# Performance work log

Hardware: AMD Instinct MI355X
Metric: run time of the kernel (lower is better)

## Reference

```python
import jax, jax.numpy as jnp
import numpy as np

D_MODEL = 128
D_STATE = 16
D_CONV = 2
EXPAND = 2
D_INNER = EXPAND * D_MODEL  # 256
DT_RANK = (D_MODEL + 15) // 16  # 8
GROUPS = 4
EPS = 1e-5


def setup_inputs() -> dict:
    key = jax.random.key(0)
    ks = jax.random.split(key, 12)
    s = lambda k, shape, sc=0.02: jax.random.normal(k, shape, dtype=jnp.float32) * sc
    inp = {
        "x_hsi": jax.random.normal(ks[0], (8, D_MODEL, 64, 64), dtype=jnp.float32),
        "W_in": s(ks[1], (D_MODEL, 2 * D_INNER)),            # in_proj (no bias)
        "conv_w": s(ks[2], (D_INNER, D_CONV), 0.5),          # depthwise causal conv, k=2
        "conv_b": s(ks[3], (D_INNER,), 0.1),
        "W_x": s(ks[4], (D_INNER, DT_RANK + 2 * D_STATE)),   # x_proj (no bias)
        "W_dt": s(ks[5], (DT_RANK, D_INNER), 0.1),
        "b_dt": s(ks[6], (D_INNER,), 0.1),
        "A_log": jnp.log(jnp.broadcast_to(jnp.arange(1, D_STATE + 1, dtype=jnp.float32), (D_INNER, D_STATE))),
        "D": jnp.ones((D_INNER,), dtype=jnp.float32),
        "W_out": s(ks[7], (D_INNER, D_MODEL)),               # out_proj (no bias)
        "gn_gamma": jnp.ones((D_MODEL,), dtype=jnp.float32),
        "gn_beta": jnp.zeros((D_MODEL,), dtype=jnp.float32),
    }
    return inp


def _causal_conv_k2(x, w, b):
    # x: [B, L, Din]; w: [Din, 2]; causal depthwise conv, kernel size 2
    xp = jnp.pad(x, ((0, 0), (1, 0), (0, 0)))
    return xp[:, :-1] * w[:, 0] + xp[:, 1:] * w[:, 1] + b


def _selective_scan(xc, dt, Bmat, Cmat, A, D):
    # xc,dt: [B,L,Din]; Bmat,Cmat: [B,L,N]; A: [Din,N]; D: [Din]
    def step(h, inp):
        dt_t, B_t, C_t, x_t = inp          # [B,Din],[B,N],[B,N],[B,Din]
        dA = jnp.exp(dt_t[..., None] * A)                      # [B,Din,N]
        dBx = dt_t[..., None] * B_t[:, None, :] * x_t[..., None]
        h = dA * h + dBx
        y = jnp.einsum('bdn,bn->bd', h, C_t)
        return h, y

    B_, L, Din = xc.shape
    h0 = jnp.zeros((B_, Din, A.shape[1]), dtype=xc.dtype)
    xs = (jnp.swapaxes(dt, 0, 1), jnp.swapaxes(Bmat, 0, 1),
          jnp.swapaxes(Cmat, 0, 1), jnp.swapaxes(xc, 0, 1))
    _, ys = jax.lax.scan(step, h0, xs)     # ys: [L,B,Din]
    return jnp.swapaxes(ys, 0, 1) + xc * D


def _mamba(x, W_in, conv_w, conv_b, W_x, W_dt, b_dt, A_log, D, W_out):
    # x: [B, L, d_model]
    xz = x @ W_in                                   # [B,L,2*Din]
    xh, z = jnp.split(xz, 2, axis=-1)
    xh = jax.nn.silu(_causal_conv_k2(xh, conv_w, conv_b))
    x_dbl = xh @ W_x                                # [B,L,dt_rank+2N]
    dt_low = x_dbl[..., :DT_RANK]
    Bmat = x_dbl[..., DT_RANK:DT_RANK + D_STATE]
    Cmat = x_dbl[..., DT_RANK + D_STATE:]
    dt = jax.nn.softplus(dt_low @ W_dt + b_dt)      # [B,L,Din]
    A = -jnp.exp(A_log)
    y = _selective_scan(xh, dt, Bmat, Cmat, A, D)
    y = y * jax.nn.silu(z)
    return y @ W_out


def _group_norm(x, gamma, beta):
    # x: [B,C,H,W]
    B_, C, H, W = x.shape
    xr = x.reshape(B_, GROUPS, -1)
    mean = xr.mean(-1, keepdims=True)
    var = xr.var(-1, keepdims=True)
    xn = ((xr - mean) * jax.lax.rsqrt(var + EPS)).reshape(B_, C, H, W)
    return xn * gamma[:, None, None] + beta[:, None, None]


def reference(x_hsi, W_in, conv_w, conv_b, W_x, W_dt, b_dt, A_log, D, W_out, gn_gamma, gn_beta):
    B_, C, H, W = x_hsi.shape
    x = jnp.transpose(x_hsi, (0, 2, 3, 1)).reshape(B_, H * W, C)
    x = _mamba(x, W_in, conv_w, conv_b, W_x, W_dt, b_dt, A_log, D, W_out)
    x = jnp.transpose(x.reshape(B_, H, W, C), (0, 3, 1, 2))
    x = jax.nn.silu(_group_norm(x, gn_gamma, gn_beta))
    return x + x_hsi
```

## Files before the change

kernel.cpp:

```cpp
#include <hip/hip_runtime.h>
#include <hip/hip_bf16.h>
#include <math.h>

#define BATCH   8
#define LSEQ    4096
#define CMODEL  128
#define DIN     256
#define NSTATE  16
#define RRANK   8
#define NCH     128
#define TCH     32

typedef __attribute__((ext_vector_type(8))) short short8;
typedef __attribute__((ext_vector_type(4))) float f32x4;
typedef __attribute__((ext_vector_type(2))) float f32x2;

__device__ __forceinline__ float sigmoid_fast(float x) {
    return __builtin_amdgcn_rcpf(1.0f + __expf(-x));
}
__device__ __forceinline__ float silu_fast(float x) { return x * sigmoid_fast(x); }
__device__ __forceinline__ float softplus_fast(float x) {
    return fmaxf(x, 0.0f) + __logf(1.0f + __expf(-fabsf(x)));
}
__device__ __forceinline__ unsigned short f2bf(float f) {
    unsigned u = __float_as_uint(f);
    return (unsigned short)((u + 0x7FFFu + ((u >> 16) & 1u)) >> 16);
}
__device__ __forceinline__ float bf2f(unsigned short u) {
    return __uint_as_float(((unsigned)u) << 16);
}
__device__ __forceinline__ unsigned pk2bf(float a, float b) {
    __hip_bfloat162 t = __float22bfloat162_rn(make_float2(a, b));
    unsigned r;
    __builtin_memcpy(&r, &t, 4);
    return r;
}

__device__ __forceinline__ void dA_powers(float dtv, const float* A, bool fast,
                                          float* dA)
{
    if (fast) {
        float e1 = __expf(dtv * A[0]);
        float e2 = e1 * e1;
        float e4 = e2 * e2;
        float e8 = e4 * e4;
        dA[0] = e1;        dA[1] = e2;        dA[2] = e2 * e1;   dA[3] = e4;
        dA[4] = e4 * e1;   dA[5] = e4 * e2;   dA[6] = e4 * dA[2]; dA[7] = e8;
        dA[8] = e8 * e1;   dA[9] = e8 * e2;   dA[10] = e8 * dA[2]; dA[11] = e8 * e4;
        dA[12] = e8 * dA[4]; dA[13] = e8 * dA[5]; dA[14] = e8 * dA[6]; dA[15] = e8 * e8;
    } else {
        #pragma unroll
        for (int n = 0; n < 16; ++n) dA[n] = __expf(dtv * A[n]);
    }
}

#define LSTR 72

__device__ __forceinline__ void tr64_bf(const float* __restrict__ src, int lds,
                                        int r0, int c0,
                                        unsigned short* __restrict__ dst, int ldd)
{
    __shared__ float ts[64][65];
    const int tid = threadIdx.x;
    #pragma unroll
    for (int it = 0; it < 4; ++it) {
        int slot = tid + it * 256;
        int i = slot >> 4, j4 = slot & 15;
        float4 v = *(const float4*)&src[(size_t)(r0 + i) * lds + c0 + j4 * 4];
        ts[i][j4*4+0] = v.x; ts[i][j4*4+1] = v.y;
        ts[i][j4*4+2] = v.z; ts[i][j4*4+3] = v.w;
    }
    __syncthreads();
    #pragma unroll
    for (int it = 0; it < 4; ++it) {
        int slot = tid + it * 256;
        int row = slot >> 4, c4 = slot & 15;
        unsigned p0 = pk2bf(ts[c4*4+0][row], ts[c4*4+1][row]);
        unsigned p1 = pk2bf(ts[c4*4+2][row], ts[c4*4+3][row]);
        unsigned long long u = (unsigned long long)p0 | ((unsigned long long)p1 << 32);
        *(unsigned long long*)&dst[(size_t)(c0 + row) * ldd + r0 + c4 * 4] = u;
    }
}

__global__ __launch_bounds__(256) void k0_setup(
    const float* __restrict__ W_in, const float* __restrict__ W_out,
    unsigned short* __restrict__ wtin, unsigned short* __restrict__ wtout,
    float* __restrict__ part)
{
    const int bid = blockIdx.x;
    if (bid < 16) {
        int ct = bid >> 3, jt = bid & 7;
        tr64_bf(W_in, 512, ct * 64, jt * 64, wtin, 128);
    } else if (bid < 24) {
        int t3 = bid - 16;
        int kt = t3 >> 1, ct = t3 & 1;
        tr64_bf(W_out, 128, kt * 64, ct * 64, wtout, 256);
    } else {
        if (threadIdx.x < 64) part[threadIdx.x] = 0.0f;
    }
}

__global__ __launch_bounds__(512) void k1_gemm_in(
    const float* __restrict__ x_hsi, const unsigned short* __restrict__ wtin,
    float* __restrict__ xh_raw, float* __restrict__ z_silu)
{
    __shared__ __align__(16) unsigned short Abf[128 * LSTR];
    __shared__ __align__(16) unsigned short Bbf[256 * LSTR];
    const int tid = threadIdx.x;
    const int R0  = blockIdx.x * 128;
    const int b   = R0 >> 12;
    const int l0  = R0 & 4095;
    const int jbase = blockIdx.y * 256;

    const int w    = tid >> 6;
    const int lane = tid & 63;
    const int lm   = lane & 15;
    const int q    = lane >> 4;
    const int mbase = (w & 1) * 64;
    const int nbase = (w >> 1) * 64;

    f32x4 acc[4][4];
    #pragma unroll
    for (int i = 0; i < 4; ++i)
        #pragma unroll
        for (int j = 0; j < 4; ++j) acc[i][j] = (f32x4){0.f, 0.f, 0.f, 0.f};

    const int cq = tid & 15;
    const int lq = tid >> 4;

    for (int kc = 0; kc < 128; kc += 64) {
        __syncthreads();
        {
            float v[4][4];
            #pragma unroll
            for (int t = 0; t < 4; ++t) {
                float4 f = *(const float4*)&x_hsi[((b * 128 + kc + cq * 4 + t) << 12) + l0 + lq * 4];
                v[t][0] = f.x; v[t][1] = f.y; v[t][2] = f.z; v[t][3] = f.w;
            }
            #pragma unroll
            for (int i = 0; i < 4; ++i) {
                unsigned p0 = pk2bf(v[0][i], v[1][i]);
                unsigned p1 = pk2bf(v[2][i], v[3][i]);
                unsigned long long u = (unsigned long long)p0 | ((unsigned long long)p1 << 32);
                *(unsigned long long*)&Abf[(lq * 4 + i) * LSTR + cq * 4] = u;
            }
        }
        #pragma unroll
        for (int it = 0; it < 4; ++it) {
            int slot = tid + it * 512;
            int r = slot >> 3, seg = slot & 7;
            short8 vb = *(const short8*)&wtin[(size_t)(jbase + r) * 128 + kc + seg * 8];
            *(short8*)&Bbf[r * LSTR + seg * 8] = vb;
        }
        __syncthreads();
        #pragma unroll
        for (int kt = 0; kt < 2; ++kt) {
            short8 af[4], bfr[4];
            #pragma unroll
            for (int mt = 0; mt < 4; ++mt)
                af[mt] = *(const short8*)&Abf[(mbase + mt * 16 + lm) * LSTR + kt * 32 + q * 8];
            #pragma unroll
            for (int nt = 0; nt < 4; ++nt)
                bfr[nt] = *(const short8*)&Bbf[(nbase + nt * 16 + lm) * LSTR + kt * 32 + q * 8];
            #pragma unroll
            for (int mt = 0; mt < 4; ++mt)
                #pragma unroll
                for (int nt = 0; nt < 4; ++nt)
                    acc[mt][nt] = __builtin_amdgcn_mfma_f32_16x16x32_bf16(
                        af[mt], bfr[nt], acc[mt][nt], 0, 0, 0);
        }
    }

    const bool is_xh = (jbase == 0);
    #pragma unroll
    for (int mt = 0; mt < 4; ++mt) {
        #pragma unroll
        for (int r = 0; r < 4; ++r) {
            int row = R0 + mbase + mt * 16 + q * 4 + r;
            #pragma unroll
            for (int nt = 0; nt < 4; ++nt) {
                int col = nbase + nt * 16 + lm;
                float val = acc[mt][nt][r];
                if (is_xh) xh_raw[row * 256 + col] = val;
                else       z_silu[row * 256 + col] = silu_fast(val);
            }
        }
    }
}

__global__ __launch_bounds__(256) void k4_xdbl(
    const float* __restrict__ xh_raw, const float* __restrict__ conv_w,
    const float* __restrict__ conv_b, const float* __restrict__ W_x,
    float* __restrict__ xdbl, unsigned short* __restrict__ xcbf)
{
    __shared__ float xcs[128][68];
    __shared__ float wxs[64 * 40];
    __shared__ float cw0[256], cw1[256], cbs[256];
    const int tid = threadIdx.x;
    cw0[tid] = conv_w[2 * tid];
    cw1[tid] = conv_w[2 * tid + 1];
    cbs[tid] = conv_b[tid];

    const int R0 = blockIdx.x * 128;
    const int tc = tid & 7;
    const int tr = tid >> 3;

    float acc[4][5];
    #pragma unroll
    for (int i = 0; i < 4; ++i)
        #pragma unroll
        for (int j = 0; j < 5; ++j) acc[i][j] = 0.0f;

    for (int kc = 0; kc < 256; kc += 64) {
        __syncthreads();
        #pragma unroll
        for (int it = 0; it < 3; ++it) {
            int i4 = tid + it * 256;
            if (i4 < 640) ((float4*)wxs)[i4] = ((const float4*)&W_x[kc * 40])[i4];
        }
        #pragma unroll
        for (int it = 0; it < 8; ++it) {
            int idx = tid + it * 256;
            int r = idx >> 4, qq = idx & 15;
            int row = R0 + r;
            float4 cur = *(const float4*)&xh_raw[row * 256 + kc + qq * 4];
            float4 prv = make_float4(0.f, 0.f, 0.f, 0.f);
            if ((row & 4095) != 0)
                prv = *(const float4*)&xh_raw[(row - 1) * 256 + kc + qq * 4];
            int d = kc + qq * 4;
            float4 o;
            o.x = silu_fast(prv.x * cw0[d+0] + cur.x * cw1[d+0] + cbs[d+0]);
            o.y = silu_fast(prv.y * cw0[d+1] + cur.y * cw1[d+1] + cbs[d+1]);
            o.z = silu_fast(prv.z * cw0[d+2] + cur.z * cw1[d+2] + cbs[d+2]);
            o.w = silu_fast(prv.w * cw0[d+3] + cur.w * cw1[d+3] + cbs[d+3]);
            *(float4*)&xcs[r][qq * 4] = o;
            unsigned p0 = pk2bf(o.x, o.y), p1 = pk2bf(o.z, o.w);
            unsigned long long u = (unsigned long long)p0 | ((unsigned long long)p1 << 32);
            *(unsigned long long*)&xcbf[(size_t)row * 256 + d] = u;
        }
        __syncthreads();
        #pragma unroll 2
        for (int k = 0; k < 64; ++k) {
            float wv[5];
            #pragma unroll
            for (int j = 0; j < 5; ++j) wv[j] = wxs[k * 40 + tc * 5 + j];
            #pragma unroll
            for (int i = 0; i < 4; ++i) {
                float a = xcs[tr * 4 + i][k];
                #pragma unroll
                for (int j = 0; j < 5; ++j) acc[i][j] = fmaf(a, wv[j], acc[i][j]);
            }
        }
    }
    #pragma unroll
    for (int i = 0; i < 4; ++i) {
        int row = R0 + tr * 4 + i;
        #pragma unroll
        for (int j = 0; j < 5; ++j) xdbl[row * 40 + tc * 5 + j] = acc[i][j];
    }
}

__global__ __launch_bounds__(256) void k6_scan1(
    const unsigned short* __restrict__ xcbf, const float* __restrict__ xdbl,
    const float* __restrict__ W_dt, const float* __restrict__ b_dt,
    const float* __restrict__ A_log,
    float* __restrict__ hend, float* __restrict__ dtsg,
    float* __restrict__ dtvg)
{
    __shared__ float xd[TCH * 40];
    const int d = threadIdx.x;
    const int chunk = blockIdx.x;
    const int b = blockIdx.y;
    const int t0 = b * LSEQ + chunk * TCH;

    {
        const float4* src = (const float4*)&xdbl[t0 * 40];
        if (d < 256) ((float4*)xd)[d] = src[d];
        int i2 = d + 256;
        if (i2 < 320) ((float4*)xd)[i2] = src[i2];
    }

    float A[16];
    #pragma unroll
    for (int qq = 0; qq < 4; ++qq) {
        float4 al = *(const float4*)&A_log[d * 16 + qq * 4];
        A[qq*4+0] = -__expf(al.x); A[qq*4+1] = -__expf(al.y);
        A[qq*4+2] = -__expf(al.z); A[qq*4+3] = -__expf(al.w);
    }
    bool fast = true;
    #pragma unroll
    for (int n = 1; n < 16; ++n)
        fast = fast && (fabsf(A[n] - (n + 1) * A[0]) <= 1e-4f * fabsf(A[n]) + 1e-7f);

    float wdt[8];
    #pragma unroll
    for (int r = 0; r < 8; ++r) wdt[r] = W_dt[r * 256 + d];
    const float bdt = b_dt[d];

    f32x2 h2[8];
    #pragma unroll
    for (int j = 0; j < 8; ++j) h2[j] = (f32x2){0.f, 0.f};
    float dtsum = 0.f;
    __syncthreads();

    #pragma unroll 2
    for (int tt = 0; tt < TCH; ++tt) {
        const int row = t0 + tt;
        float xcv = bf2f(xcbf[(size_t)row * 256 + d]);

        const float* xr = &xd[tt * 40];
        float dl[8];
        *(float4*)&dl[0] = *(const float4*)&xr[0];
        *(float4*)&dl[4] = *(const float4*)&xr[4];
        float dtr = bdt;
        #pragma unroll
        for (int r = 0; r < 8; ++r) dtr = fmaf(dl[r], wdt[r], dtr);
        float dtv = softplus_fast(dtr);
        dtsum += dtv;
        float dtx = dtv * xcv;
        dtvg[(size_t)row * 256 + d] = dtv;

        float Bt[16] __attribute__((aligned(16)));
        #pragma unroll
        for (int qq = 0; qq < 4; ++qq)
            *(float4*)&Bt[qq * 4] = *(const float4*)&xr[8 + qq * 4];

        float dA[16] __attribute__((aligned(16)));
        dA_powers(dtv, A, fast, dA);
        const f32x2* dA2 = (const f32x2*)dA;
        const f32x2* Bt2 = (const f32x2*)Bt;
        f32x2 dtx2 = (f32x2){dtx, dtx};
        #pragma unroll
        for (int j = 0; j < 8; ++j)
            h2[j] = dA2[j] * h2[j] + dtx2 * Bt2[j];
    }

    const float* hf = (const float*)h2;
    const int base = ((b * NCH + chunk) * 256 + d) * 16;
    #pragma unroll
    for (int qq = 0; qq < 4; ++qq)
        *(float4*)&hend[base + qq * 4] = make_float4(hf[qq*4], hf[qq*4+1], hf[qq*4+2], hf[qq*4+3]);
    dtsg[(b * NCH + chunk) * 256 + d] = dtsum;
}

__global__ __launch_bounds__(256) void k7_combine(
    const float* __restrict__ dtsg, const float* __restrict__ A_log,
    float* __restrict__ hx)
{
    const int idx = blockIdx.x * 256 + threadIdx.x;
    const int b = idx >> 12;
    const int rem = idx & 4095;
    const int d = rem >> 4, n = rem & 15;
    const float An = -__expf(A_log[d * 16 + n]);
    const int base = b * NCH * 4096 + rem;
    const int sbase = b * NCH * 256 + d;
    float h = 0.f;
    float Sb[8], Eb[8];
    #pragma unroll
    for (int j = 0; j < 8; ++j) {
        Sb[j] = dtsg[sbase + j * 256];
        Eb[j] = hx[base + j * 4096];
    }
    for (int g = 0; g < NCH / 8; ++g) {
        const int o  = base + g * 32768;
        const int so = sbase + g * 2048;
        float Sn[8] = {0,0,0,0,0,0,0,0}, En[8] = {0,0,0,0,0,0,0,0};
        if (g < NCH / 8 - 1) {
            #pragma unroll
            for (int j = 0; j < 8; ++j) {
                Sn[j] = dtsg[so + 2048 + j * 256];
                En[j] = hx[o + 32768 + j * 4096];
            }
        }
        #pragma unroll
        for (int j = 0; j < 8; ++j) {
            hx[o + j * 4096] = h;
            float P = __expf(Sb[j] * An);
            h = fmaf(P, h, Eb[j]);
        }
        #pragma unroll
        for (int j = 0; j < 8; ++j) { Sb[j] = Sn[j]; Eb[j] = En[j]; }
    }
}

__global__ __launch_bounds__(256) void k8_scan2(
    const unsigned short* __restrict__ xcbf, const float* __restrict__ xdbl,
    const float* __restrict__ dtvg, const float* __restrict__ A_log,
    const float* __restrict__ Dvec, const float* __restrict__ hin,
    const float* __restrict__ zsilu, unsigned short* __restrict__ ybf)
{
    __shared__ float xd[TCH * 40];
    const int d = threadIdx.x;
    const int chunk = blockIdx.x;
    const int b = blockIdx.y;
    const int t0 = b * LSEQ + chunk * TCH;

    {
        const float4* src = (const float4*)&xdbl[t0 * 40];
        if (d < 256) ((float4*)xd)[d] = src[d];
        int i2 = d + 256;
        if (i2 < 320) ((float4*)xd)[i2] = src[i2];
    }

    float A[16];
    #pragma unroll
    for (int qq = 0; qq < 4; ++qq) {
        float4 al = *(const float4*)&A_log[d * 16 + qq * 4];
        A[qq*4+0] = -__expf(al.x); A[qq*4+1] = -__expf(al.y);
        A[qq*4+2] = -__expf(al.z); A[qq*4+3] = -__expf(al.w);
    }
    bool fast = true;
    #pragma unroll
    for (int n = 1; n < 16; ++n)
        fast = fast && (fabsf(A[n] - (n + 1) * A[0]) <= 1e-4f * fabsf(A[n]) + 1e-7f);

    const float Dd = Dvec[d];

    f32x2 h2[8];
    const int hbase = ((b * NCH + chunk) * 256 + d) * 16;
    {
        float hf[16];
        #pragma unroll
        for (int qq = 0; qq < 4; ++qq) {
            float4 hv = *(const float4*)&hin[hbase + qq * 4];
            hf[qq*4+0] = hv.x; hf[qq*4+1] = hv.y; hf[qq*4+2] = hv.z; hf[qq*4+3] = hv.w;
        }
        #pragma unroll
        for (int j = 0; j < 8; ++j) h2[j] = (f32x2){hf[2*j], hf[2*j+1]};
    }
    __syncthreads();

    #pragma unroll 2
    for (int tt = 0; tt < TCH; ++tt) {
        const int row = t0 + tt;
        const size_t gi = (size_t)row * 256 + d;
        float dtv = dtvg[gi];
        float xcv = bf2f(xcbf[gi]);
        float dtx = dtv * xcv;

        const float* xr = &xd[tt * 40];
        float Bt[16] __attribute__((aligned(16)));
        float Ct[16] __attribute__((aligned(16)));
        #pragma unroll
        for (int qq = 0; qq < 4; ++qq) {
            *(float4*)&Bt[qq * 4] = *(const float4*)&xr[8 + qq * 4];
            *(float4*)&Ct[qq * 4] = *(const float4*)&xr[24 + qq * 4];
        }

        float dA[16] __attribute__((aligned(16)));
        dA_powers(dtv, A, fast, dA);
        const f32x2* dA2 = (const f32x2*)dA;
        const f32x2* Bt2 = (const f32x2*)Bt;
        const f32x2* Ct2 = (const f32x2*)Ct;
        f32x2 dtx2 = (f32x2){dtx, dtx};
        f32x2 yv2 = (f32x2){0.f, 0.f};
        #pragma unroll
        for (int j = 0; j < 8; ++j) {
            h2[j] = dA2[j] * h2[j] + dtx2 * Bt2[j];
            yv2 = yv2 + h2[j] * Ct2[j];
        }
        float yv = yv2.x + yv2.y;
        yv = fmaf(Dd, xcv, yv);
        ybf[gi] = f2bf(yv * zsilu[gi]);
    }
}

__global__ __launch_bounds__(256) void k9_gemm_out(
    const unsigned short* __restrict__ ybf, const unsigned short* __restrict__ wtout,
    unsigned short* __restrict__ out_bf, float* __restrict__ part)
{
    __shared__ __align__(16) unsigned short Abf[128 * LSTR];
    __shared__ __align__(16) unsigned short Bbf[128 * LSTR];
    const int tid = threadIdx.x;
    const int R0 = blockIdx.x * 128;
    const int b  = R0 >> 12;
    const int l0 = R0 & 4095;

    const int w    = tid >> 6;
    const int lane = tid & 63;
    const int lm   = lane & 15;
    const int q    = lane >> 4;
    const int mbase = (w & 1) * 64;
    const int nbase = (w >> 1) * 64;

    f32x4 acc[4][4];
    #pragma unroll
    for (int i = 0; i < 4; ++i)
        #pragma unroll
        for (int j = 0; j < 4; ++j) acc[i][j] = (f32x4){0.f, 0.f, 0.f, 0.f};

    for (int kc = 0; kc < 256; kc += 64) {
        __syncthreads();
        #pragma unroll
        for (int it = 0; it < 4; ++it) {
            int slot = tid + it * 256;
            int r = slot >> 3, seg = slot & 7;
            short8 va = *(const short8*)&wtout[(size_t)r * 256 + kc + seg * 8];
            *(short8*)&Abf[r * LSTR + seg * 8] = va;
            short8 vb = *(const short8*)&ybf[(size_t)(R0 + r) * 256 + kc + seg * 8];
            *(short8*)&Bbf[r * LSTR + seg * 8] = vb;
        }
        __syncthreads();
        #pragma unroll
        for (int kt = 0; kt < 2; ++kt) {
            short8 af[4], bfr[4];
            #pragma unroll
            for (int mt = 0; mt < 4; ++mt)
                af[mt] = *(const short8*)&Abf[(mbase + mt * 16 + lm) * LSTR + kt * 32 + q * 8];
            #pragma unroll
            for (int nt = 0; nt < 4; ++nt)
                bfr[nt] = *(const short8*)&Bbf[(nbase + nt * 16 + lm) * LSTR + kt * 32 + q * 8];
            #pragma unroll
            for (int mt = 0; mt < 4; ++mt)
                #pragma unroll
                for (int nt = 0; nt < 4; ++nt)
                    acc[mt][nt] = __builtin_amdgcn_mfma_f32_16x16x32_bf16(
                        af[mt], bfr[nt], acc[mt][nt], 0, 0, 0);
        }
    }

    #pragma unroll
    for (int mt = 0; mt < 4; ++mt) {
        #pragma unroll
        for (int r = 0; r < 4; ++r) {
            int c = mbase + mt * 16 + q * 4 + r;
            long base = (long)(b * 128 + c) * 4096 + l0;
            #pragma unroll
            for (int nt = 0; nt < 4; ++nt)
                out_bf[base + nbase + nt * 16 + lm] = f2bf(acc[mt][nt][r]);
        }
    }

    float s0 = 0.f, q0 = 0.f, s1 = 0.f, q1 = 0.f;
    #pragma unroll
    for (int mt = 0; mt < 4; ++mt)
        #pragma unroll
        for (int nt = 0; nt < 4; ++nt)
            #pragma unroll
            for (int r = 0; r < 4; ++r) {
                float v = acc[mt][nt][r];
                if (mt < 2) { s0 += v; q0 += v * v; }
                else        { s1 += v; q1 += v * v; }
            }
    #pragma unroll
    for (int off = 32; off > 0; off >>= 1) {
        s0 += __shfl_down(s0, off, 64);
        q0 += __shfl_down(q0, off, 64);
        s1 += __shfl_down(s1, off, 64);
        q1 += __shfl_down(q1, off, 64);
    }
    if (lane == 0) {
        int g0 = mbase >> 5;
        atomicAdd(&part[(b * 4 + g0) * 2],     s0);
        atomicAdd(&part[(b * 4 + g0) * 2 + 1], q0);
        atomicAdd(&part[(b * 4 + g0 + 1) * 2],     s1);
        atomicAdd(&part[(b * 4 + g0 + 1) * 2 + 1], q1);
    }
}

__global__ __launch_bounds__(256) void k10c_apply(
    const unsigned short* __restrict__ out_bf, const float* __restrict__ part,
    const float* __restrict__ gamma, const float* __restrict__ beta,
    const float* __restrict__ x_hsi, float* __restrict__ out)
{
    __shared__ float sstat[64];
    if (threadIdx.x < 32) {
        float S = part[threadIdx.x * 2];
        float Q = part[threadIdx.x * 2 + 1];
        const float inv_n = 1.0f / 131072.0f;
        float mean = S * inv_n;
        float var  = Q * inv_n - mean * mean;
        sstat[threadIdx.x * 2]     = mean;
        sstat[threadIdx.x * 2 + 1] = rsqrtf(var + 1e-5f);
    }
    __syncthreads();
    const int idx4 = blockIdx.x * 256 + threadIdx.x;
    const int flat = idx4 * 4;
    const int c = (flat >> 12) & 127;
    const int b = flat >> 19;
    const int g = c >> 5;
    const float mean = sstat[(b * 4 + g) * 2];
    const float inv  = sstat[(b * 4 + g) * 2 + 1];
    const float ga = gamma[c], be = beta[c];
    ushort4 u = *(const ushort4*)&out_bf[flat];
    float4 r = *(const float4*)&x_hsi[flat];
    float vv[4] = {bf2f(u.x), bf2f(u.y), bf2f(u.z), bf2f(u.w)};
    float rr[4] = {r.x, r.y, r.z, r.w};
    float o[4];
    #pragma unroll
    for (int qq = 0; qq < 4; ++qq) {
        float xn = (vv[qq] - mean) * inv;
        float gv = xn * ga + be;
        o[qq] = silu_fast(gv) + rr[qq];
    }
    *(float4*)&out[flat] = make_float4(o[0], o[1], o[2], o[3]);
}

extern "C" void kernel_launch(void* const* d_in, const int* in_sizes, int n_in,
                              void* d_out, int out_size, void* d_ws, size_t ws_size,
                              hipStream_t stream)
{
    const float* x_hsi  = (const float*)d_in[0];
    const float* W_in   = (const float*)d_in[1];
    const float* conv_w = (const float*)d_in[2];
    const float* conv_b = (const float*)d_in[3];
    const float* W_x    = (const float*)d_in[4];
    const float* W_dt   = (const float*)d_in[5];
    const float* b_dt   = (const float*)d_in[6];
    const float* A_log  = (const float*)d_in[7];
    const float* Dv     = (const float*)d_in[8];
    const float* W_out  = (const float*)d_in[9];
    const float* gnw    = (const float*)d_in[10];
    const float* gnb    = (const float*)d_in[11];

    float* ws = (float*)d_ws;
    float* xh_raw = ws + 0;
    float* zsilu  = ws + 8388608;
    float* xdbl   = ws + 16777216;
    float* hx     = ws + 17104896;
    float* dtvg   = ws + 21299200;
    float* dtsg   = ws + 29687808;
    unsigned short* xcbf = (unsigned short*)(ws + 29949952);
    unsigned short* out_bf = (unsigned short*)(ws + 34144256);
    float* part   = ws + 36241408;
    unsigned short* wtin  = (unsigned short*)(ws + 36241536);
    unsigned short* wtout = (unsigned short*)(ws + 36274304);
    unsigned short* ybf   = (unsigned short*)xh_raw;
    float* outp   = (float*)d_out;

    k0_setup<<<25, 256, 0, stream>>>(W_in, W_out, wtin, wtout, part);
    k1_gemm_in<<<dim3(256, 2), 512, 0, stream>>>(x_hsi, wtin, xh_raw, zsilu);
    k4_xdbl<<<256, 256, 0, stream>>>(xh_raw, conv_w, conv_b, W_x, xdbl, xcbf);
    k6_scan1<<<dim3(NCH, BATCH), 256, 0, stream>>>(xcbf, xdbl, W_dt, b_dt, A_log,
                                                   hx, dtsg, dtvg);
    k7_combine<<<128, 256, 0, stream>>>(dtsg, A_log, hx);
    k8_scan2<<<dim3(NCH, BATCH), 256, 0, stream>>>(xcbf, xdbl, dtvg,
                                                   A_log, Dv, hx, zsilu, ybf);
    k9_gemm_out<<<256, 256, 0, stream>>>(ybf, wtout, out_bf, part);
    k10c_apply<<<4096, 256, 0, stream>>>(out_bf, part, gnw, gnb, x_hsi, outp);
}
```

Measured before the change: 236.5 us.

## Store intermediates in bf16/fp16 to cut memory traffic between kernels

The in-projection outputs (xh and silu(z)) are now written as bf16 instead of fp32, the per-step dt values are stored as fp16, and the B/C rows staged in shared memory are packed to bf16 in both scan kernels. All consumers are updated to unpack these formats, and the workspace layout shrinks accordingly. The aim is to roughly halve global memory traffic for the largest intermediates in this bandwidth-bound pipeline. The cost is reduced precision in the scan inputs (dt, B, C, x) and the gating values, which could affect accuracy tolerance.

```diff
diff --git a/kernel.cpp b/kernel.cpp
--- a/kernel.cpp
+++ b/kernel.cpp
@@ -1,5 +1,6 @@
 #include <hip/hip_runtime.h>
 #include <hip/hip_bf16.h>
+#include <hip/hip_fp16.h>
 #include <math.h>
 
 #define BATCH   8
@@ -22,10 +23,6 @@
 __device__ __forceinline__ float softplus_fast(float x) {
     return fmaxf(x, 0.0f) + __logf(1.0f + __expf(-fabsf(x)));
 }
-__device__ __forceinline__ unsigned short f2bf(float f) {
-    unsigned u = __float_as_uint(f);
-    return (unsigned short)((u + 0x7FFFu + ((u >> 16) & 1u)) >> 16);
-}
 __device__ __forceinline__ float bf2f(unsigned short u) {
     return __uint_as_float(((unsigned)u) << 16);
 }
@@ -35,22 +32,27 @@
     __builtin_memcpy(&r, &t, 4);
     return r;
 }
-
-__device__ __forceinline__ void dA_powers(float dtv, const float* A, bool fast,
-                                          float* dA)
+__device__ __forceinline__ unsigned short f2bf1(float v) {
+    return (unsigned short)pk2bf(v, v);
+}
+__device__ __forceinline__ f32x2 up2(unsigned w) {
+    return (f32x2){ __uint_as_float(w << 16), __uint_as_float(w & 0xffff0000u) };
+}
+
+__device__ __forceinline__ void dA_powers2(float dtv, const float* A, bool fast,
+                                           f32x2* dA2)
 {
     if (fast) {
         float e1 = __expf(dtv * A[0]);
         float e2 = e1 * e1;
-        float e4 = e2 * e2;
-        float e8 = e4 * e4;
-        dA[0] = e1;        dA[1] = e2;        dA[2] = e2 * e1;   dA[3] = e4;
-        dA[4] = e4 * e1;   dA[5] = e4 * e2;   dA[6] = e4 * dA[2]; dA[7] = e8;
-        dA[8] = e8 * e1;   dA[9] = e8 * e2;   dA[10] = e8 * dA[2]; dA[11] = e8 * e4;
-        dA[12] = e8 * dA[4]; dA[13] = e8 * dA[5]; dA[14] = e8 * dA[6]; dA[15] = e8 * e8;
+        dA2[0] = (f32x2){e1, e2};
+        f32x2 e2s = (f32x2){e2, e2};
+        #pragma unroll
+        for (int j = 1; j < 8; ++j) dA2[j] = dA2[j-1] * e2s;
     } else {
         #pragma unroll
-        for (int n = 0; n < 16; ++n) dA[n] = __expf(dtv * A[n]);
+        for (int j = 0; j < 8; ++j)
+            dA2[j] = (f32x2){__expf(dtv * A[2*j]), __expf(dtv * A[2*j+1])};
     }
 }
 
@@ -102,7 +104,7 @@
 
 __global__ __launch_bounds__(512) void k1_gemm_in(
     const float* __restrict__ x_hsi, const unsigned short* __restrict__ wtin,
-    float* __restrict__ xh_raw, float* __restrict__ z_silu)
+    unsigned short* __restrict__ xhbf, unsigned short* __restrict__ zbf)
 {
     __shared__ __align__(16) unsigned short Abf[128 * LSTR];
     __shared__ __align__(16) unsigned short Bbf[256 * LSTR];
@@ -181,15 +183,15 @@
             for (int nt = 0; nt < 4; ++nt) {
                 int col = nbase + nt * 16 + lm;
                 float val = acc[mt][nt][r];
-                if (is_xh) xh_raw[row * 256 + col] = val;
-                else       z_silu[row * 256 + col] = silu_fast(val);
+                if (is_xh) xhbf[row * 256 + col] = f2bf1(val);
+                else       zbf[row * 256 + col]  = f2bf1(silu_fast(val));
             }
         }
     }
 }
 
 __global__ __launch_bounds__(256) void k4_xdbl(
-    const float* __restrict__ xh_raw, const float* __restrict__ conv_w,
+    const unsigned short* __restrict__ xhbf, const float* __restrict__ conv_w,
     const float* __restrict__ conv_b, const float* __restrict__ W_x,
     float* __restrict__ xdbl, unsigned short* __restrict__ xcbf)
 {
@@ -223,18 +225,21 @@
             int idx = tid + it * 256;
             int r = idx >> 4, qq = idx & 15;
             int row = R0 + r;
-            float4 cur = *(const float4*)&xh_raw[row * 256 + kc + qq * 4];
-            float4 prv = make_float4(0.f, 0.f, 0.f, 0.f);
-            if ((row & 4095) != 0)
-                prv = *(const float4*)&xh_raw[(row - 1) * 256 + kc + qq * 4];
+            ushort4 cu = *(const ushort4*)&xhbf[(size_t)row * 256 + kc + qq * 4];
+            float cur[4] = {bf2f(cu.x), bf2f(cu.y), bf2f(cu.z), bf2f(cu.w)};
+            float pv[4] = {0.f, 0.f, 0.f, 0.f};
+            if ((row & 4095) != 0) {
+                ushort4 pu = *(const ushort4*)&xhbf[(size_t)(row - 1) * 256 + kc + qq * 4];
+                pv[0] = bf2f(pu.x); pv[1] = bf2f(pu.y);
+                pv[2] = bf2f(pu.z); pv[3] = bf2f(pu.w);
+            }
             int d = kc + qq * 4;
-            float4 o;
-            o.x = silu_fast(prv.x * cw0[d+0] + cur.x * cw1[d+0] + cbs[d+0]);
-            o.y = silu_fast(prv.y * cw0[d+1] + cur.y * cw1[d+1] + cbs[d+1]);
-            o.z = silu_fast(prv.z * cw0[d+2] + cur.z * cw1[d+2] + cbs[d+2]);
-            o.w = silu_fast(prv.w * cw0[d+3] + cur.w * cw1[d+3] + cbs[d+3]);
-            *(float4*)&xcs[r][qq * 4] = o;
-            unsigned p0 = pk2bf(o.x, o.y), p1 = pk2bf(o.z, o.w);
+            float o[4];
+            #pragma unroll
+            for (int e = 0; e < 4; ++e)
+                o[e] = silu_fast(pv[e] * cw0[d+e] + cur[e] * cw1[d+e] + cbs[d+e]);
+            *(float4*)&xcs[r][qq * 4] = make_float4(o[0], o[1], o[2], o[3]);
+            unsigned p0 = pk2bf(o[0], o[1]), p1 = pk2bf(o[2], o[3]);
             unsigned long long u = (unsigned long long)p0 | ((unsigned long long)p1 << 32);
             *(unsigned long long*)&xcbf[(size_t)row * 256 + d] = u;
         }
@@ -265,19 +270,24 @@
     const float* __restrict__ W_dt, const float* __restrict__ b_dt,
     const float* __restrict__ A_log,
     float* __restrict__ hend, float* __restrict__ dtsg,
-    float* __restrict__ dtvg)
-{
-    __shared__ float xd[TCH * 40];
+    __half* __restrict__ dtvh)
+{
+    __shared__ __align__(16) unsigned char xdb[TCH * 64];
     const int d = threadIdx.x;
     const int chunk = blockIdx.x;
     const int b = blockIdx.y;
     const int t0 = b * LSEQ + chunk * TCH;
 
     {
-        const float4* src = (const float4*)&xdbl[t0 * 40];
-        if (d < 256) ((float4*)xd)[d] = src[d];
-        int i2 = d + 256;
-        if (i2 < 320) ((float4*)xd)[i2] = src[i2];
+        int row = d >> 3, seg = d & 7;
+        const float4* src = (const float4*)&xdbl[(size_t)(t0 + row) * 40];
+        if (seg < 2) {
+            *(float4*)&xdb[row * 64 + seg * 16] = src[seg];
+        } else if (seg < 6) {
+            float4 f = src[seg];
+            unsigned p0 = pk2bf(f.x, f.y), p1 = pk2bf(f.z, f.w);
+            *(uint2*)&xdb[row * 64 + 32 + (seg - 2) * 8] = make_uint2(p0, p1);
+        }
     }
 
     float A[16];
@@ -308,27 +318,25 @@
         const int row = t0 + tt;
         float xcv = bf2f(xcbf[(size_t)row * 256 + d]);
 
-        const float* xr = &xd[tt * 40];
+        const unsigned char* xr = &xdb[tt * 64];
         float dl[8];
-        *(float4*)&dl[0] = *(const float4*)&xr[0];
-        *(float4*)&dl[4] = *(const float4*)&xr[4];
+        *(float4*)&dl[0] = *(const float4*)xr;
+        *(float4*)&dl[4] = *(const float4*)(xr + 16);
         float dtr = bdt;
         #pragma unroll
         for (int r = 0; r < 8; ++r) dtr = fmaf(dl[r], wdt[r], dtr);
         float dtv = softplus_fast(dtr);
         dtsum += dtv;
         float dtx = dtv * xcv;
-        dtvg[(size_t)row * 256 + d] = dtv;
-
-        float Bt[16] __attribute__((aligned(16)));
-        #pragma unroll
-        for (int qq = 0; qq < 4; ++qq)
-            *(float4*)&Bt[qq * 4] = *(const float4*)&xr[8 + qq * 4];
-
-        float dA[16] __attribute__((aligned(16)));
-        dA_powers(dtv, A, fast, dA);
-        const f32x2* dA2 = (const f32x2*)dA;
-        const f32x2* Bt2 = (const f32x2*)Bt;
+        dtvh[(size_t)row * 256 + d] = __float2half(dtv);
+
+        uint4 bu0 = *(const uint4*)(xr + 32);
+        uint4 bu1 = *(const uint4*)(xr + 48);
+        f32x2 Bt2[8] = {up2(bu0.x), up2(bu0.y), up2(bu0.z), up2(bu0.w),
+                        up2(bu1.x), up2(bu1.y), up2(bu1.z), up2(bu1.w)};
+
+        f32x2 dA2[8];
+        dA_powers2(dtv, A, fast, dA2);
         f32x2 dtx2 = (f32x2){dtx, dtx};
         #pragma unroll
         for (int j = 0; j < 8; ++j)
@@ -385,21 +393,21 @@
 
 __global__ __launch_bounds__(256) void k8_scan2(
     const unsigned short* __restrict__ xcbf, const float* __restrict__ xdbl,
-    const float* __restrict__ dtvg, const float* __restrict__ A_log,
+    const __half* __restrict__ dtvh, const float* __restrict__ A_log,
     const float* __restrict__ Dvec, const float* __restrict__ hin,
-    const float* __restrict__ zsilu, unsigned short* __restrict__ ybf)
-{
-    __shared__ float xd[TCH * 40];
+    const unsigned short* __restrict__ zbf, unsigned short* __restrict__ ybf)
+{
+    __shared__ __align__(16) unsigned char xdb[TCH * 64];
     const int d = threadIdx.x;
     const int chunk = blockIdx.x;
     const int b = blockIdx.y;
     const int t0 = b * LSEQ + chunk * TCH;
 
     {
-        const float4* src = (const float4*)&xdbl[t0 * 40];
-        if (d < 256) ((float4*)xd)[d] = src[d];
-        int i2 = d + 256;
-        if (i2 < 320) ((float4*)xd)[i2] = src[i2];
+        int row = d >> 3, seg = d & 7;
+        float4 f = *(const float4*)&xdbl[(size_t)(t0 + row) * 40 + 8 + seg * 4];
+        unsigned p0 = pk2bf(f.x, f.y), p1 = pk2bf(f.z, f.w);
+        *(uint2*)&xdb[row * 64 + seg * 8] = make_uint2(p0, p1);
     }
 
     float A[16];
@@ -434,24 +442,22 @@
     for (int tt = 0; tt < TCH; ++tt) {
         const int row = t0 + tt;
         const size_t gi = (size_t)row * 256 + d;
-        float dtv = dtvg[gi];
+        float dtv = __half2float(dtvh[gi]);
         float xcv = bf2f(xcbf[gi]);
         float dtx = dtv * xcv;
 
-        const float* xr = &xd[tt * 40];
-        float Bt[16] __attribute__((aligned(16)));
-        float Ct[16] __attribute__((aligned(16)));
-        #pragma unroll
-        for (int qq = 0; qq < 4; ++qq) {
-            *(float4*)&Bt[qq * 4] = *(const float4*)&xr[8 + qq * 4];
-            *(float4*)&Ct[qq * 4] = *(const float4*)&xr[24 + qq * 4];
-        }
-
-        float dA[16] __attribute__((aligned(16)));
-        dA_powers(dtv, A, fast, dA);
-        const f32x2* dA2 = (const f32x2*)dA;
-        const f32x2* Bt2 = (const f32x2*)Bt;
-        const f32x2* Ct2 = (const f32x2*)Ct;
+        const unsigned char* xr = &xdb[tt * 64];
+        uint4 bu0 = *(const uint4*)(xr + 0);
+        uint4 bu1 = *(const uint4*)(xr + 16);
+        uint4 cu0 = *(const uint4*)(xr + 32);
+        uint4 cu1 = *(const uint4*)(xr + 48);
+        f32x2 Bt2[8] = {up2(bu0.x), up2(bu0.y), up2(bu0.z), up2(bu0.w),
+                        up2(bu1.x), up2(bu1.y), up2(bu1.z), up2(bu1.w)};
+        f32x2 Ct2[8] = {up2(cu0.x), up2(cu0.y), up2(cu0.z), up2(cu0.w),
+                        up2(cu1.x), up2(cu1.y), up2(cu1.z), up2(cu1.w)};
+
+        f32x2 dA2[8];
+        dA_powers2(dtv, A, fast, dA2);
         f32x2 dtx2 = (f32x2){dtx, dtx};
         f32x2 yv2 = (f32x2){0.f, 0.f};
         #pragma unroll
@@ -461,7 +467,7 @@
         }
         float yv = yv2.x + yv2.y;
         yv = fmaf(Dd, xcv, yv);
-        ybf[gi] = f2bf(yv * zsilu[gi]);
+        ybf[gi] = f2bf1(yv * bf2f(zbf[gi]));
     }
 }
 
@@ -527,7 +533,7 @@
             long base = (long)(b * 128 + c) * 4096 + l0;
             #pragma unroll
             for (int nt = 0; nt < 4; ++nt)
-                out_bf[base + nbase + nt * 16 + lm] = f2bf(acc[mt][nt][r]);
+                out_bf[base + nbase + nt * 16 + lm] = f2bf1(acc[mt][nt][r]);
         }
     }
 
@@ -614,28 +620,28 @@
     const float* gnb    = (const float*)d_in[11];
 
     float* ws = (float*)d_ws;
-    float* xh_raw = ws + 0;
-    float* zsilu  = ws + 8388608;
-    float* xdbl   = ws + 16777216;
-    float* hx     = ws + 17104896;
-    float* dtvg   = ws + 21299200;
-    float* dtsg   = ws + 29687808;
-    unsigned short* xcbf = (unsigned short*)(ws + 29949952);
-    unsigned short* out_bf = (unsigned short*)(ws + 34144256);
-    float* part   = ws + 36241408;
-    unsigned short* wtin  = (unsigned short*)(ws + 36241536);
-    unsigned short* wtout = (unsigned short*)(ws + 36274304);
-    unsigned short* ybf   = (unsigned short*)xh_raw;
+    unsigned short* xhbf = (unsigned short*)(ws + 0);
+    unsigned short* zbf  = (unsigned short*)(ws + 4194304);
+    float* xdbl   = ws + 8388608;
+    float* hx     = ws + 8716288;
+    __half* dtvh  = (__half*)(ws + 12910592);
+    float* dtsg   = ws + 17104896;
+    unsigned short* xcbf   = (unsigned short*)(ws + 17367040);
+    unsigned short* out_bf = (unsigned short*)(ws + 21561344);
+    float* part   = ws + 23658496;
+    unsigned short* wtin  = (unsigned short*)(ws + 23658624);
+    unsigned short* wtout = (unsigned short*)(ws + 23691392);
+    unsigned short* ybf   = xhbf;
     float* outp   = (float*)d_out;
 
     k0_setup<<<25, 256, 0, stream>>>(W_in, W_out, wtin, wtout, part);
-    k1_gemm_in<<<dim3(256, 2), 512, 0, stream>>>(x_hsi, wtin, xh_raw, zsilu);
-    k4_xdbl<<<256, 256, 0, stream>>>(xh_raw, conv_w, conv_b, W_x, xdbl, xcbf);
+    k1_gemm_in<<<dim3(256, 2), 512, 0, stream>>>(x_hsi, wtin, xhbf, zbf);
+    k4_xdbl<<<256, 256, 0, stream>>>(xhbf, conv_w, conv_b, W_x, xdbl, xcbf);
     k6_scan1<<<dim3(NCH, BATCH), 256, 0, stream>>>(xcbf, xdbl, W_dt, b_dt, A_log,
-                                                   hx, dtsg, dtvg);
+                                                   hx, dtsg, dtvh);
     k7_combine<<<128, 256, 0, stream>>>(dtsg, A_log, hx);
-    k8_scan2<<<dim3(NCH, BATCH), 256, 0, stream>>>(xcbf, xdbl, dtvg,
-                                                   A_log, Dv, hx, zsilu, ybf);
+    k8_scan2<<<dim3(NCH, BATCH), 256, 0, stream>>>(xcbf, xdbl, dtvh,
+                                                   A_log, Dv, hx, zbf, ybf);
     k9_gemm_out<<<256, 256, 0, stream>>>(ybf, wtout, out_bf, part);
     k10c_apply<<<4096, 256, 0, stream>>>(out_bf, part, gnw, gnb, x_hsi, outp);
 }
```

New measurement: 232.9 us. About the same (-1.5%).
